# Optimization experiments

Measured on AMD Instinct MI355X. Metric: run time of the kernel, lower is better.

Reference implementation:

```python
import jax, jax.numpy as jnp
import numpy as np

B, L, D, H = 1, 2048, 1024, 16
d = D // H  # head dim = 64


def setup_inputs() -> dict:
    key = jax.random.key(0)
    ks = jax.random.split(key, 8)
    s = 1.0 / np.sqrt(D)
    return {
        "x": jax.random.normal(ks[0], (B, L, D), jnp.float32),
        "Wqkv_w": (jax.random.normal(ks[1], (D, 3 * D), jnp.float32) * s),
        "Wqkv_b": jnp.zeros((3 * D,), jnp.float32),
        "out_w": (jax.random.normal(ks[2], (D, D), jnp.float32) * s),
        "out_b": jnp.zeros((D,), jnp.float32),
        "W_static": jnp.zeros((H, d, d), jnp.float32),
        "Lambda_raw": jax.random.uniform(ks[3], (H, d, d), jnp.float32, -3.0, 3.0),
        "Gamma": jax.random.uniform(ks[4], (H, d, d), jnp.float32, -0.5 / np.sqrt(d), 0.5 / np.sqrt(d)),
        "gate_w1": (jax.random.normal(ks[5], (D, D // 2), jnp.float32) * s),
        "gate_b1": jnp.zeros((D // 2,), jnp.float32),
        "gate_w2": (jax.random.normal(ks[6], (D // 2, H), jnp.float32) * (1.0 / np.sqrt(D // 2))),
        "gate_b2": jnp.zeros((H,), jnp.float32),
    }


def _forward(x, Wqkv_w, Wqkv_b, out_w, out_b, W_static, Lambda_raw, Gamma,
             gate_w1, gate_b1, gate_w2, gate_b2):
    Bb, Ll, Dm = x.shape
    Hh = Gamma.shape[0]
    dd = Dm // Hh
    scale = 1.0 / np.sqrt(dd)

    # qkv projection: (B,L,3D) -> (3, B, H, L, d) layout
    qkv = (x @ Wqkv_w + Wqkv_b).reshape(Bb, Ll, 3, Hh, dd)
    q = jnp.transpose(qkv[:, :, 0], (0, 2, 1, 3))  # (B,H,L,d)
    k = jnp.transpose(qkv[:, :, 1], (0, 2, 1, 3))
    v = jnp.transpose(qkv[:, :, 2], (0, 2, 1, 3))

    # --- softmax branch (causal, additive -10000 mask like the original) ---
    scores = jnp.einsum('bhid,bhjd->bhij', q, k) * scale
    causal_mask = jnp.triu(jnp.full((Ll, Ll), -10000.0, dtype=scores.dtype), 1)
    attn = jax.nn.softmax(scores + causal_mask, axis=-1)
    y_softmax = jnp.einsum('bhij,bhjd->bhid', attn, v)

    # --- STP branch: linear recurrence over time via lax.scan ---
    retention = 1.0 - jax.nn.sigmoid(Lambda_raw)  # (H,d,d)
    k_stp = k * scale

    def step(state, inp):
        q_t, k_t, v_t = inp  # each (B,H,d)
        hebbian = v_t[..., :, None] * k_t[..., None, :]          # (B,H,d,d)
        state = retention * state + Gamma * hebbian              # (B,H,d,d)
        y_t = jnp.einsum('bhij,bhj->bhi', W_static + state, q_t)  # (B,H,d)
        return state, y_t

    state0 = jnp.zeros((Bb, Hh, dd, dd), x.dtype)
    qT = jnp.moveaxis(q, 2, 0)      # (L,B,H,d)
    kT = jnp.moveaxis(k_stp, 2, 0)
    vT = jnp.moveaxis(v, 2, 0)
    _, ys = jax.lax.scan(step, state0, (qT, kT, vT))
    y_stp = jnp.moveaxis(ys, 0, 2)  # (B,H,L,d)

    # --- learned gate: Linear -> GELU(exact) -> Linear -> sigmoid ---
    g = jax.nn.gelu(x @ gate_w1 + gate_b1, approximate=False)
    alpha = jax.nn.sigmoid(g @ gate_w2 + gate_b2)        # (B,L,H)
    alpha = jnp.transpose(alpha, (0, 2, 1))[..., None]   # (B,H,L,1)

    y = alpha * y_softmax + (1.0 - alpha) * y_stp        # (B,H,L,d)
    y = jnp.transpose(y, (0, 2, 1, 3)).reshape(Bb, Ll, Dm)
    return y @ out_w + out_b


def reference(x, Wqkv_w, Wqkv_b, out_w, out_b, W_static, Lambda_raw, Gamma,
              gate_w1, gate_b1, gate_w2, gate_b2):
    return _forward(x, Wqkv_w, Wqkv_b, out_w, out_b, W_static, Lambda_raw,
                    Gamma, gate_w1, gate_b1, gate_w2, gate_b2)
```

## Files before the change

kernel.cpp:

```cpp
#include <hip/hip_runtime.h>
#include <hip/hip_bf16.h>

#define L_SEQ 2048
#define DMODEL 1024
#define NHEAD 16
#define DHEAD 64
#define D3 3072

typedef __attribute__((ext_vector_type(8))) short s8v;
typedef __attribute__((ext_vector_type(4))) float f4v;
typedef unsigned int u32;
#define AS1 __attribute__((address_space(1)))
#define AS3 __attribute__((address_space(3)))

__device__ __forceinline__ short f2bf(float f) {
  __hip_bfloat16 h = __float2bfloat16(f);
  return *reinterpret_cast<short*>(&h);
}
__device__ __forceinline__ float bf2f(short s) {
  return __uint_as_float(((u32)(unsigned short)s) << 16);
}
__device__ __forceinline__ int pack2bf(float lo, float hi) {
  return (int)(((unsigned)(unsigned short)f2bf(hi) << 16) |
               (unsigned)(unsigned short)f2bf(lo));
}

__device__ __forceinline__ void transpose32(const float* __restrict__ W,
    short* __restrict__ Wt, int K, int N, int bx, int by, int tid)
{
  __shared__ float T[32][33];
  int col = tid & 31, rb = tid >> 5;
  #pragma unroll
  for (int it = 0; it < 4; ++it) {
    int r = it * 8 + rb;
    T[r][col] = W[(size_t)(by * 32 + r) * N + bx * 32 + col];
  }
  __syncthreads();
  #pragma unroll
  for (int it = 0; it < 4; ++it) {
    int r = it * 8 + rb;
    Wt[(size_t)(bx * 32 + r) * K + by * 32 + col] = f2bf(T[col][r]);
  }
}

__global__ __launch_bounds__(256) void prep_kernel(
    const float* __restrict__ x, short* __restrict__ xb,
    const float* __restrict__ Wqkv_w, const float* __restrict__ gw1,
    const float* __restrict__ out_w, short* __restrict__ wt_buf,
    short* __restrict__ wtO)
{
  int b = blockIdx.x, tid = threadIdx.x;
  if (b < 2048) {
    int i = (b * 256 + tid) * 4;
    float4 v = *(const float4*)(x + i);
    short4 o;
    o.x = f2bf(v.x); o.y = f2bf(v.y); o.z = f2bf(v.z); o.w = f2bf(v.w);
    *(short4*)(xb + i) = o;
  } else if (b < 5120) {
    int r = b - 2048;
    transpose32(Wqkv_w, wt_buf, 1024, 3072, r % 96, r / 96, tid);
  } else if (b < 5632) {
    int r = b - 5120;
    transpose32(gw1, wt_buf + 3072 * 1024, 1024, 512, r % 16, r / 16, tid);
  } else {
    int r = b - 5632;
    transpose32(out_w, wtO, 1024, 1024, r % 32, r / 32, tid);
  }
}

template<int BM, int BN, int MODE>
__global__ __launch_bounds__(256, 6) void gemm_mfma(
    const short* __restrict__ A, const short* __restrict__ Bt,
    const float* __restrict__ bias, const float* __restrict__ bias2,
    float* __restrict__ C, short* __restrict__ C2,
    short* __restrict__ QbP, short* __restrict__ KbP,
    int M, int N, int K)
{
  constexpr int LA = BM / 64, LB = BN / 64;
  constexpr int WM = BM / 2, WN = BN / 2;
  constexpr int MT = WM / 16, NT = WN / 16;
  __shared__ __align__(16) short As[2][BM * 32];
  __shared__ __align__(16) short Bs[2][BN * 32];
  const int tid = threadIdx.x;
  const int w = tid >> 6, lane = tid & 63;
  const int quad = lane >> 4, c = lane & 15;
  const int m0 = blockIdx.y * BM, n0 = blockIdx.x * BN;
  const int wm = (w & 1) * WM, wn = (w >> 1) * WN;
  f4v acc[MT][NT] = {};

  auto stage = [&](int buf, int k0) {
    #pragma unroll
    for (int it = 0; it < LA; ++it) {
      int off = (it * 256 + tid) * 16;
      int row = off >> 6, colh = (off & 63) >> 1;
      __builtin_amdgcn_global_load_lds(
          (const AS1 u32*)(A + (size_t)(m0 + row) * K + k0 + colh),
          (AS3 u32*)(&As[buf][0] + (off >> 1)), 16, 0, 0);
    }
    #pragma unroll
    for (int it = 0; it < LB; ++it) {
      int off = (it * 256 + tid) * 16;
      int row = off >> 6, colh = (off & 63) >> 1;
      __builtin_amdgcn_global_load_lds(
          (const AS1 u32*)(Bt + (size_t)(n0 + row) * K + k0 + colh),
          (AS3 u32*)(&Bs[buf][0] + (off >> 1)), 16, 0, 0);
    }
  };
  stage(0, 0);
  int cur = 0;
  for (int k0 = 0; k0 < K; k0 += 32) {
    __syncthreads();
    if (k0 + 32 < K) stage(cur ^ 1, k0 + 32);
    s8v af[MT], bf[NT];
    #pragma unroll
    for (int mt = 0; mt < MT; ++mt)
      af[mt] = *(s8v*)&As[cur][(wm + mt * 16 + c) * 32 + quad * 8];
    #pragma unroll
    for (int nt = 0; nt < NT; ++nt)
      bf[nt] = *(s8v*)&Bs[cur][(wn + nt * 16 + c) * 32 + quad * 8];
    #pragma unroll
    for (int mt = 0; mt < MT; ++mt)
      #pragma unroll
      for (int nt = 0; nt < NT; ++nt)
        acc[mt][nt] = __builtin_amdgcn_mfma_f32_16x16x32_bf16(
            af[mt], bf[nt], acc[mt][nt], 0, 0, 0);
    cur ^= 1;
  }
  #pragma unroll
  for (int mt = 0; mt < MT; ++mt)
    #pragma unroll
    for (int r = 0; r < 4; ++r) {
      int m = m0 + wm + mt * 16 + quad * 4 + r;
      #pragma unroll
      for (int nt = 0; nt < NT; ++nt) {
        int n = n0 + wn + nt * 16 + c;
        float v = acc[mt][nt][r];
        if (MODE == 0) {
          C[(size_t)m * N + n] = v + bias[n];
        } else {
          if (n < 2048) {
            float v2 = v + bias[n];
            int hh = (n >> 6) & 15, ee = n & 63;
            short* dst = (n < 1024) ? QbP : KbP;
            dst[((size_t)hh * 2048 + m) * 64 + ee] = f2bf(v2);
          } else if (n < 3072) {
            C[(size_t)m * 1024 + (n - 2048)] = v + bias[n];
          } else {
            float t = v + bias2[n - 3072];
            t = 0.5f * t * (1.0f + erff(t * 0.70710678118654752f));
            C2[(size_t)m * 512 + (n - 3072)] = f2bf(t);
          }
        }
      }
    }
}

__global__ __launch_bounds__(256) void attn_mfma(
    const short* __restrict__ Qb, const short* __restrict__ Kb,
    const short* __restrict__ Vtb, float* __restrict__ O0,
    float* __restrict__ O1, float* __restrict__ ml)
{
  const int bid = blockIdx.x;
  int h, qt, ts, te;
  float *Odst, *mdst, *ldst;
  if (bid < 512) {
    qt = 31 - (bid >> 5);
    int r = bid & 31; h = r >> 1;
    int n = qt + 1, n2 = (n + 1) >> 1;
    if ((r & 1) == 0) {
      ts = 0; te = n2;
      int s = h * 32 + qt;
      Odst = O0 + (size_t)s * 4096; mdst = ml + s * 64; ldst = ml + 32768 + s * 64;
    } else {
      ts = n2; te = n;
      int s = h * 16 + (qt - 16);
      Odst = O1 + (size_t)s * 4096; mdst = ml + 65536 + s * 64; ldst = ml + 81920 + s * 64;
    }
  } else {
    int r = bid - 512; qt = 15 - (r >> 4); h = r & 15; ts = 0; te = qt + 1;
    int s = h * 32 + qt;
    Odst = O0 + (size_t)s * 4096; mdst = ml + s * 64; ldst = ml + 32768 + s * 64;
  }
  const int q0 = qt * 64;
  const int tid = threadIdx.x;
  const int w = tid >> 6, lane = tid & 63;
  const int quad = lane >> 4, c = lane & 15;

  __shared__ __align__(16) char smem[27648];
  short* Ks = (short*)smem;
  short* Vt = Ks + 4608;
  short* Ps = Vt + 4608;
  float* Ob = (float*)smem;

  const int qrow = q0 + w * 16 + c;
  s8v qf[2];
  qf[0] = *(const s8v*)(Qb + ((size_t)h * 2048 + qrow) * 64 + quad * 8);
  qf[1] = *(const s8v*)(Qb + ((size_t)h * 2048 + qrow) * 64 + 32 + quad * 8);

  const int srow = tid >> 3, sc = (tid & 7) * 8;
  int4 pk0, pk1, pv0, pv1;
  auto load_tile = [&](int t0) {
    const short* kbase = Kb + ((size_t)h * 2048 + t0 * 64) * 64;
    const short* vbase = Vtb + (size_t)h * 64 * 2048 + t0 * 64;
    pk0 = *(const int4*)(kbase + (size_t)srow * 64 + sc);
    pk1 = *(const int4*)(kbase + (size_t)(srow + 32) * 64 + sc);
    pv0 = *(const int4*)(vbase + (size_t)srow * 2048 + sc);
    pv1 = *(const int4*)(vbase + (size_t)(srow + 32) * 2048 + sc);
  };
  load_tile(ts);

  f4v o_acc[4] = {};
  float m = -1e30f, l = 0.f;

  for (int t0 = ts; t0 < te; ++t0) {
    __syncthreads();
    *(int4*)&Ks[srow * 72 + sc] = pk0;
    *(int4*)&Ks[(srow + 32) * 72 + sc] = pk1;
    *(int4*)&Vt[srow * 72 + sc] = pv0;
    *(int4*)&Vt[(srow + 32) * 72 + sc] = pv1;
    __syncthreads();
    if (t0 + 1 < te) load_tile(t0 + 1);

    f4v s_acc[4] = {};
    #pragma unroll
    for (int kt = 0; kt < 4; ++kt) {
      #pragma unroll
      for (int kc = 0; kc < 2; ++kc) {
        s8v kf = *(s8v*)&Ks[(kt * 16 + c) * 72 + kc * 32 + quad * 8];
        s_acc[kt] = __builtin_amdgcn_mfma_f32_16x16x32_bf16(kf, qf[kc], s_acc[kt], 0, 0, 0);
      }
    }
    float sv[4][4];
    bool full = (t0 * 64 + 63) <= (q0 + w * 16);
    #pragma unroll
    for (int kt = 0; kt < 4; ++kt)
      #pragma unroll
      for (int r = 0; r < 4; ++r) {
        float s = s_acc[kt][r] * 0.125f;
        if (!full) {
          int key = t0 * 64 + kt * 16 + quad * 4 + r;
          s = (key <= qrow) ? s : -1e30f;
        }
        sv[kt][r] = s;
      }
    float mloc = -1e30f;
    #pragma unroll
    for (int kt = 0; kt < 4; ++kt)
      #pragma unroll
      for (int r = 0; r < 4; ++r) mloc = fmaxf(mloc, sv[kt][r]);
    mloc = fmaxf(mloc, __shfl_xor(mloc, 16));
    mloc = fmaxf(mloc, __shfl_xor(mloc, 32));
    float mnew = fmaxf(fmaxf(m, mloc), -1e20f);
    float alpha = __expf(m - mnew);
    m = mnew;
    float p[4][4], ls = 0.f;
    #pragma unroll
    for (int kt = 0; kt < 4; ++kt)
      #pragma unroll
      for (int r = 0; r < 4; ++r) { p[kt][r] = __expf(sv[kt][r] - mnew); ls += p[kt][r]; }
    ls += __shfl_xor(ls, 16);
    ls += __shfl_xor(ls, 32);
    l = l * alpha + ls;
    #pragma unroll
    for (int mt = 0; mt < 4; ++mt)
      #pragma unroll
      for (int r = 0; r < 4; ++r) o_acc[mt][r] *= alpha;
    short* Pw = Ps + w * 1152;
    #pragma unroll
    for (int kt = 0; kt < 4; ++kt) {
      *(int*)&Pw[c * 72 + kt * 16 + quad * 4]     = pack2bf(p[kt][0], p[kt][1]);
      *(int*)&Pw[c * 72 + kt * 16 + quad * 4 + 2] = pack2bf(p[kt][2], p[kt][3]);
    }
    #pragma unroll
    for (int kc2 = 0; kc2 < 2; ++kc2) {
      s8v pf = *(s8v*)&Pw[c * 72 + kc2 * 32 + quad * 8];
      #pragma unroll
      for (int mt = 0; mt < 4; ++mt) {
        s8v vf = *(s8v*)&Vt[(mt * 16 + c) * 72 + kc2 * 32 + quad * 8];
        o_acc[mt] = __builtin_amdgcn_mfma_f32_16x16x32_bf16(vf, pf, o_acc[mt], 0, 0, 0);
      }
    }
  }

  __syncthreads();
  #pragma unroll
  for (int mt = 0; mt < 4; ++mt)
    #pragma unroll
    for (int r = 0; r < 4; ++r)
      Ob[(w * 16 + c) * 66 + mt * 16 + quad * 4 + r] = o_acc[mt][r];
  if (quad == 0) { mdst[w * 16 + c] = m; ldst[w * 16 + c] = l; }
  __syncthreads();
  for (int i = tid; i < 4096; i += 256)
    Odst[i] = Ob[(i >> 6) * 66 + (i & 63)];
}

__global__ __launch_bounds__(256) void attn_merge(
    const float* __restrict__ O0, const float* __restrict__ O1,
    const float* __restrict__ ml, const float* __restrict__ ystp,
    const float* __restrict__ alpha, short* __restrict__ ycb)
{
  int bid = blockIdx.x;
  int h = bid >> 5, qt = bid & 31;
  int slot0 = h * 32 + qt;
  int tid = threadIdx.x;
  for (int it = 0; it < 16; ++it) {
    int idx = it * 256 + tid;
    int q = idx >> 6, e = idx & 63;
    int gq = qt * 64 + q;
    float oo = O0[(size_t)slot0 * 4096 + idx];
    float m0v = ml[slot0 * 64 + q], l0v = ml[32768 + slot0 * 64 + q];
    float ll;
    if (qt >= 16) {
      int slot1 = h * 16 + (qt - 16);
      float o1 = O1[(size_t)slot1 * 4096 + idx];
      float m1v = ml[65536 + slot1 * 64 + q], l1v = ml[81920 + slot1 * 64 + q];
      float ms = fmaxf(m0v, m1v);
      float w0 = __expf(m0v - ms), w1 = __expf(m1v - ms);
      oo = oo * w0 + o1 * w1;
      ll = l0v * w0 + l1v * w1;
    } else {
      ll = l0v;
    }
    float ys = oo / ll;
    float a = alpha[gq * 16 + h];
    float yst = ystp[((size_t)h * 2048 + gq) * 64 + e];
    ycb[(size_t)gq * 1024 + h * 64 + e] = f2bf(a * ys + (1.f - a) * yst);
  }
}

__global__ __launch_bounds__(256) void stp_local(const float* __restrict__ Vf,
    const short* __restrict__ Kb, const float* __restrict__ Lam,
    const float* __restrict__ Gam, float* __restrict__ states,
    short* __restrict__ Vtb)
{
  int c = blockIdx.x, h = blockIdx.y;
  int tid = threadIdx.x;
  int i = tid >> 2, j0 = (tid & 3) * 16;
  __shared__ float Kc[64][64];
  __shared__ float Vc[64][65];
  for (int idx = tid; idx < 1024; idx += 256) {
    int t = idx >> 4, e4 = (idx & 15) * 4;
    short4 ks = *(const short4*)(Kb + ((size_t)h * 2048 + c * 64 + t) * 64 + e4);
    Kc[t][e4]     = bf2f(ks.x) * 0.125f;
    Kc[t][e4 + 1] = bf2f(ks.y) * 0.125f;
    Kc[t][e4 + 2] = bf2f(ks.z) * 0.125f;
    Kc[t][e4 + 3] = bf2f(ks.w) * 0.125f;
    float4 vv = *(const float4*)(Vf + (size_t)(c * 64 + t) * 1024 + h * 64 + e4);
    Vc[t][e4] = vv.x; Vc[t][e4 + 1] = vv.y; Vc[t][e4 + 2] = vv.z; Vc[t][e4 + 3] = vv.w;
  }
  float r[16], g[16], s[16];
  #pragma unroll
  for (int e = 0; e < 16; ++e) {
    int idx = h * 4096 + i * 64 + j0 + e;
    r[e] = 1.f / (1.f + expf(Lam[idx]));
    g[e] = Gam[idx];
    s[e] = 0.f;
  }
  __syncthreads();
  for (int idx = tid; idx < 2048; idx += 256) {
    int dim = idx >> 5, k2 = idx & 31;
    *(int*)&Vtb[((size_t)h * 64 + dim) * 2048 + c * 64 + k2 * 2] =
        pack2bf(Vc[k2 * 2][dim], Vc[k2 * 2 + 1][dim]);
  }
  for (int t = 0; t < 64; ++t) {
    float v = Vc[t][i];
    #pragma unroll
    for (int e = 0; e < 16; ++e)
      s[e] = r[e] * s[e] + g[e] * (v * Kc[t][j0 + e]);
  }
  #pragma unroll
  for (int e = 0; e < 16; ++e)
    states[((size_t)h * 32 + c) * 4096 + i * 64 + j0 + e] = s[e];
}

__global__ __launch_bounds__(256) void stp_scan(const float* __restrict__ Lam,
                                                float* __restrict__ states)
{
  int gid = blockIdx.x * 256 + threadIdx.x;
  float r = 1.f / (1.f + expf(Lam[gid]));
  float r64 = r;
  #pragma unroll
  for (int q = 0; q < 6; ++q) r64 *= r64;
  int h = gid >> 12, low = gid & 4095;
  const size_t base = (size_t)h * 32 * 4096 + low;
  float v[32];
  #pragma unroll
  for (int c = 0; c < 32; ++c) v[c] = states[base + (size_t)c * 4096];
  float acc = 0.f;
  #pragma unroll
  for (int c = 0; c < 32; ++c) {
    float d = v[c];
    v[c] = acc;
    acc = r64 * acc + d;
  }
  #pragma unroll
  for (int c = 0; c < 32; ++c) states[base + (size_t)c * 4096] = v[c];
}

__global__ __launch_bounds__(256) void stp_out(const float* __restrict__ Vf,
    const short* __restrict__ Kb, const short* __restrict__ Qb,
    const float* __restrict__ Lam, const float* __restrict__ Gam,
    const float* __restrict__ Wst, const float* __restrict__ states,
    float* __restrict__ ystp)
{
  int c = blockIdx.x, h = blockIdx.y;
  int tid = threadIdx.x;
  int i = tid >> 2, j0 = (tid & 3) * 16;
  __shared__ float Kc[64][64];
  __shared__ float Vc[64][64];
  __shared__ float Qc[64][64];
  for (int idx = tid; idx < 1024; idx += 256) {
    int t = idx >> 4, e4 = (idx & 15) * 4;
    size_t bo = ((size_t)h * 2048 + c * 64 + t) * 64 + e4;
    short4 ks = *(const short4*)(Kb + bo);
    short4 qs = *(const short4*)(Qb + bo);
    Kc[t][e4]     = bf2f(ks.x) * 0.125f;
    Kc[t][e4 + 1] = bf2f(ks.y) * 0.125f;
    Kc[t][e4 + 2] = bf2f(ks.z) * 0.125f;
    Kc[t][e4 + 3] = bf2f(ks.w) * 0.125f;
    Qc[t][e4]     = bf2f(qs.x);
    Qc[t][e4 + 1] = bf2f(qs.y);
    Qc[t][e4 + 2] = bf2f(qs.z);
    Qc[t][e4 + 3] = bf2f(qs.w);
    float4 vv = *(const float4*)(Vf + (size_t)(c * 64 + t) * 1024 + h * 64 + e4);
    Vc[t][e4] = vv.x; Vc[t][e4 + 1] = vv.y; Vc[t][e4 + 2] = vv.z; Vc[t][e4 + 3] = vv.w;
  }
  float r[16], g[16], s[16], w[16];
  #pragma unroll
  for (int e = 0; e < 16; ++e) {
    int idx = h * 4096 + i * 64 + j0 + e;
    r[e] = 1.f / (1.f + expf(Lam[idx]));
    g[e] = Gam[idx];
    w[e] = Wst[idx];
    s[e] = states[((size_t)h * 32 + c) * 4096 + i * 64 + j0 + e];
  }
  __syncthreads();
  for (int t = 0; t < 64; ++t) {
    float v = Vc[t][i];
    float y = 0.f;
    #pragma unroll
    for (int e = 0; e < 16; ++e) {
      s[e] = r[e] * s[e] + g[e] * (v * Kc[t][j0 + e]);
      y += (w[e] + s[e]) * Qc[t][j0 + e];
    }
    y += __shfl_xor(y, 1);
    y += __shfl_xor(y, 2);
    if ((tid & 3) == 0)
      ystp[((size_t)h * L_SEQ + c * 64 + t) * 64 + i] = y;
  }
}

__global__ __launch_bounds__(256) void gate2_kernel(const short* __restrict__ g_bf,
    const float* __restrict__ w2, const float* __restrict__ b2,
    float* __restrict__ alpha)
{
  int tid = threadIdx.x;
  int gid = blockIdx.x * 16 + (tid >> 4);
  int sub = tid & 15;
  int l = gid >> 4, h = gid & 15;
  const short* grow = g_bf + (size_t)l * 512 + sub * 32;
  float acc = 0.f;
  #pragma unroll
  for (int c2 = 0; c2 < 32; c2 += 2) {
    u32 pk = *(const u32*)(grow + c2);
    float g0 = __uint_as_float(pk << 16);
    float g1 = __uint_as_float(pk & 0xffff0000u);
    int cb = sub * 32 + c2;
    acc += g0 * w2[cb * 16 + h] + g1 * w2[(cb + 1) * 16 + h];
  }
  acc += __shfl_xor(acc, 1);
  acc += __shfl_xor(acc, 2);
  acc += __shfl_xor(acc, 4);
  acc += __shfl_xor(acc, 8);
  if (sub == 0) alpha[gid] = 1.f / (1.f + expf(-(acc + b2[h])));
}

extern "C" void kernel_launch(void* const* d_in, const int* in_sizes, int n_in,
                              void* d_out, int out_size, void* d_ws, size_t ws_size,
                              hipStream_t stream) {
  (void)in_sizes; (void)n_in; (void)out_size; (void)ws_size;
  const float* x      = (const float*)d_in[0];
  const float* Wqkv_w = (const float*)d_in[1];
  const float* Wqkv_b = (const float*)d_in[2];
  const float* out_w  = (const float*)d_in[3];
  const float* out_b  = (const float*)d_in[4];
  const float* W_st   = (const float*)d_in[5];
  const float* Lam    = (const float*)d_in[6];
  const float* Gam    = (const float*)d_in[7];
  const float* gw1    = (const float*)d_in[8];
  const float* gb1    = (const float*)d_in[9];
  const float* gw2    = (const float*)d_in[10];
  const float* gb2    = (const float*)d_in[11];

  float* ws     = (float*)d_ws;
  float* Vf     = ws;
  float* O0buf  = ws + 2097152;
  float* ystp   = ws + 4194304;
  float* states = ws + 6291456;
  float* ovl    = ws + 8388608;
  float* alpha  = ws + 12058624;
  float* ml     = ws + 12091392;
  short* Qb     = (short*)(ws + 12189696);
  short* Kb     = Qb + 2097152;
  short* wtO    = (short*)(ws + 14286848);
  short* xb     = (short*)ovl;
  short* wt_buf = (short*)(ovl + 1048576);
  short* g_bf   = (short*)(ovl + 2883584);
  short* Vtb    = (short*)ovl;
  float* O1buf  = states;
  short* ycb    = (short*)(states + 1048576);

  prep_kernel<<<dim3(6656), 256, 0, stream>>>(x, xb, Wqkv_w, gw1, out_w, wt_buf, wtO);
  gemm_mfma<64, 64, 2><<<dim3(56, 32), 256, 0, stream>>>(
      xb, wt_buf, Wqkv_b, gb1, Vf, g_bf, Qb, Kb, 2048, 3584, 1024);
  gate2_kernel<<<dim3(2048), 256, 0, stream>>>(g_bf, gw2, gb2, alpha);
  stp_local<<<dim3(32, 16), 256, 0, stream>>>(Vf, Kb, Lam, Gam, states, Vtb);
  stp_scan<<<dim3(256), 256, 0, stream>>>(Lam, states);
  stp_out<<<dim3(32, 16), 256, 0, stream>>>(Vf, Kb, Qb, Lam, Gam, W_st, states, ystp);
  attn_mfma<<<dim3(768), 256, 0, stream>>>(Qb, Kb, Vtb, O0buf, O1buf, ml);
  attn_merge<<<dim3(512), 256, 0, stream>>>(O0buf, O1buf, ml, ystp, alpha, ycb);
  gemm_mfma<64, 64, 0><<<dim3(16, 32), 256, 0, stream>>>(
      ycb, wtO, out_b, nullptr, (float*)d_out, nullptr, nullptr, nullptr, 2048, 1024, 1024);
}
```

Before: 277.2 us.

## Split attention key range into up to three pieces and split-K the output GEMM

```diff
diff --git a/kernel.cpp b/kernel.cpp
--- a/kernel.cpp
+++ b/kernel.cpp
@@ -84,7 +84,17 @@
   const int tid = threadIdx.x;
   const int w = tid >> 6, lane = tid & 63;
   const int quad = lane >> 4, c = lane & 15;
-  const int m0 = blockIdx.y * BM, n0 = blockIdx.x * BN;
+  int n0, kb, ke;
+  size_t cofs = 0;
+  if (MODE == 3) {
+    n0 = (blockIdx.x & 15) * BN;
+    int kh = blockIdx.x >> 4;
+    kb = kh * (K / 2); ke = kb + K / 2;
+    cofs = (size_t)kh * M * N;
+  } else {
+    n0 = blockIdx.x * BN; kb = 0; ke = K;
+  }
+  const int m0 = blockIdx.y * BM;
   const int wm = (w & 1) * WM, wn = (w >> 1) * WN;
   f4v acc[MT][NT] = {};
 
@@ -106,11 +116,11 @@
           (AS3 u32*)(&Bs[buf][0] + (off >> 1)), 16, 0, 0);
     }
   };
-  stage(0, 0);
+  stage(0, kb);
   int cur = 0;
-  for (int k0 = 0; k0 < K; k0 += 32) {
+  for (int k0 = kb; k0 < ke; k0 += 32) {
     __syncthreads();
-    if (k0 + 32 < K) stage(cur ^ 1, k0 + 32);
+    if (k0 + 32 < ke) stage(cur ^ 1, k0 + 32);
     s8v af[MT], bf[NT];
     #pragma unroll
     for (int mt = 0; mt < MT; ++mt)
@@ -135,8 +145,8 @@
       for (int nt = 0; nt < NT; ++nt) {
         int n = n0 + wn + nt * 16 + c;
         float v = acc[mt][nt][r];
-        if (MODE == 0) {
-          C[(size_t)m * N + n] = v + bias[n];
+        if (MODE == 3) {
+          C[cofs + (size_t)m * N + n] = v;
         } else {
           if (n < 2048) {
             float v2 = v + bias[n];
@@ -155,32 +165,42 @@
     }
 }
 
+__global__ __launch_bounds__(256) void splitk_add(const float* __restrict__ Cp,
+    const float* __restrict__ bias, float* __restrict__ out)
+{
+  int i = (blockIdx.x * 256 + threadIdx.x) * 4;
+  float4 a = *(const float4*)(Cp + i);
+  float4 b = *(const float4*)(Cp + 2097152 + i);
+  float4 bs = *(const float4*)(bias + (i & 1023));
+  float4 o;
+  o.x = a.x + b.x + bs.x; o.y = a.y + b.y + bs.y;
+  o.z = a.z + b.z + bs.z; o.w = a.w + b.w + bs.w;
+  *(float4*)(out + i) = o;
+}
+
+__device__ __forceinline__ int piece_slot(int qt, int h, int p) {
+  if (qt >= 16) return (qt - 16) * 48 + h * 3 + p;
+  if (qt >= 8)  return 768 + (qt - 8) * 32 + h * 2 + p;
+  return 1024 + qt * 16 + h;
+}
+
 __global__ __launch_bounds__(256) void attn_mfma(
     const short* __restrict__ Qb, const short* __restrict__ Kb,
-    const short* __restrict__ Vtb, float* __restrict__ O0,
-    float* __restrict__ O1, float* __restrict__ ml)
+    const short* __restrict__ Vtb, float* __restrict__ Opart,
+    float* __restrict__ mpart, float* __restrict__ lpart)
 {
   const int bid = blockIdx.x;
-  int h, qt, ts, te;
-  float *Odst, *mdst, *ldst;
-  if (bid < 512) {
-    qt = 31 - (bid >> 5);
-    int r = bid & 31; h = r >> 1;
-    int n = qt + 1, n2 = (n + 1) >> 1;
-    if ((r & 1) == 0) {
-      ts = 0; te = n2;
-      int s = h * 32 + qt;
-      Odst = O0 + (size_t)s * 4096; mdst = ml + s * 64; ldst = ml + 32768 + s * 64;
-    } else {
-      ts = n2; te = n;
-      int s = h * 16 + (qt - 16);
-      Odst = O1 + (size_t)s * 4096; mdst = ml + 65536 + s * 64; ldst = ml + 81920 + s * 64;
-    }
-  } else {
-    int r = bid - 512; qt = 15 - (r >> 4); h = r & 15; ts = 0; te = qt + 1;
-    int s = h * 32 + qt;
-    Odst = O0 + (size_t)s * 4096; mdst = ml + s * 64; ldst = ml + 32768 + s * 64;
-  }
+  int h, qt, p, np;
+  if (bid < 768)       { int j = bid;        qt = 31 - j / 48; int r = j % 48; h = r / 3; p = r % 3; np = 3; }
+  else if (bid < 1024) { int j = bid - 768;  qt = 15 - j / 32; int r = j % 32; h = r >> 1; p = r & 1; np = 2; }
+  else                 { int j = bid - 1024; qt = 7 - (j >> 4); h = j & 15; p = 0; np = 1; }
+  const int n = qt + 1;
+  const int ts = (p * n) / np, te = ((p + 1) * n) / np;
+  const int ps = piece_slot(qt, h, p);
+  float* Odst = Opart + (size_t)ps * 4096;
+  float* mdst = mpart + ps * 64;
+  float* ldst = lpart + ps * 64;
+
   const int q0 = qt * 64;
   const int tid = threadIdx.x;
   const int w = tid >> 6, lane = tid & 63;
@@ -253,11 +273,11 @@
     float mnew = fmaxf(fmaxf(m, mloc), -1e20f);
     float alpha = __expf(m - mnew);
     m = mnew;
-    float p[4][4], ls = 0.f;
+    float pv[4][4], ls = 0.f;
     #pragma unroll
     for (int kt = 0; kt < 4; ++kt)
       #pragma unroll
-      for (int r = 0; r < 4; ++r) { p[kt][r] = __expf(sv[kt][r] - mnew); ls += p[kt][r]; }
+      for (int r = 0; r < 4; ++r) { pv[kt][r] = __expf(sv[kt][r] - mnew); ls += pv[kt][r]; }
     ls += __shfl_xor(ls, 16);
     ls += __shfl_xor(ls, 32);
     l = l * alpha + ls;
@@ -268,8 +288,8 @@
     short* Pw = Ps + w * 1152;
     #pragma unroll
     for (int kt = 0; kt < 4; ++kt) {
-      *(int*)&Pw[c * 72 + kt * 16 + quad * 4]     = pack2bf(p[kt][0], p[kt][1]);
-      *(int*)&Pw[c * 72 + kt * 16 + quad * 4 + 2] = pack2bf(p[kt][2], p[kt][3]);
+      *(int*)&Pw[c * 72 + kt * 16 + quad * 4]     = pack2bf(pv[kt][0], pv[kt][1]);
+      *(int*)&Pw[c * 72 + kt * 16 + quad * 4 + 2] = pack2bf(pv[kt][2], pv[kt][3]);
     }
     #pragma unroll
     for (int kc2 = 0; kc2 < 2; ++kc2) {
@@ -295,31 +315,27 @@
 }
 
 __global__ __launch_bounds__(256) void attn_merge(
-    const float* __restrict__ O0, const float* __restrict__ O1,
-    const float* __restrict__ ml, const float* __restrict__ ystp,
+    const float* __restrict__ Opart, const float* __restrict__ mpart,
+    const float* __restrict__ lpart, const float* __restrict__ ystp,
     const float* __restrict__ alpha, short* __restrict__ ycb)
 {
   int bid = blockIdx.x;
   int h = bid >> 5, qt = bid & 31;
-  int slot0 = h * 32 + qt;
+  int np = (qt >= 16) ? 3 : ((qt >= 8) ? 2 : 1);
+  int ps0 = piece_slot(qt, h, 0);
   int tid = threadIdx.x;
   for (int it = 0; it < 16; ++it) {
     int idx = it * 256 + tid;
     int q = idx >> 6, e = idx & 63;
     int gq = qt * 64 + q;
-    float oo = O0[(size_t)slot0 * 4096 + idx];
-    float m0v = ml[slot0 * 64 + q], l0v = ml[32768 + slot0 * 64 + q];
-    float ll;
-    if (qt >= 16) {
-      int slot1 = h * 16 + (qt - 16);
-      float o1 = O1[(size_t)slot1 * 4096 + idx];
-      float m1v = ml[65536 + slot1 * 64 + q], l1v = ml[81920 + slot1 * 64 + q];
-      float ms = fmaxf(m0v, m1v);
-      float w0 = __expf(m0v - ms), w1 = __expf(m1v - ms);
-      oo = oo * w0 + o1 * w1;
-      ll = l0v * w0 + l1v * w1;
-    } else {
-      ll = l0v;
+    float ms = mpart[ps0 * 64 + q];
+    for (int p2 = 1; p2 < np; ++p2)
+      ms = fmaxf(ms, mpart[(ps0 + p2) * 64 + q]);
+    float oo = 0.f, ll = 0.f;
+    for (int p2 = 0; p2 < np; ++p2) {
+      float wp = __expf(mpart[(ps0 + p2) * 64 + q] - ms);
+      oo += Opart[(size_t)(ps0 + p2) * 4096 + idx] * wp;
+      ll += lpart[(ps0 + p2) * 64 + q] * wp;
     }
     float ys = oo / ll;
     float a = alpha[gq * 16 + h];
@@ -494,21 +510,21 @@
 
   float* ws     = (float*)d_ws;
   float* Vf     = ws;
-  float* O0buf  = ws + 2097152;
-  float* ystp   = ws + 4194304;
-  float* states = ws + 6291456;
-  float* ovl    = ws + 8388608;
-  float* alpha  = ws + 12058624;
-  float* ml     = ws + 12091392;
-  short* Qb     = (short*)(ws + 12189696);
-  short* Kb     = Qb + 2097152;
-  short* wtO    = (short*)(ws + 14286848);
-  short* xb     = (short*)ovl;
-  short* wt_buf = (short*)(ovl + 1048576);
-  short* g_bf   = (short*)(ovl + 2883584);
-  short* Vtb    = (short*)ovl;
-  float* O1buf  = states;
-  short* ycb    = (short*)(states + 1048576);
+  float* ystp   = ws + 2097152;
+  float* states = ws + 4194304;
+  short* xb     = (short*)(ws + 6291456);
+  short* wt_buf = (short*)(ws + 7340032);
+  short* g_bf   = (short*)(ws + 9175040);
+  float* alpha  = ws + 9699328;
+  short* Qb     = (short*)(ws + 9732096);
+  short* Kb     = (short*)(ws + 10780672);
+  short* wtO    = (short*)(ws + 11829248);
+  short* Vtb    = (short*)(ws + 12353536);
+  short* ycb    = (short*)(ws + 13402112);
+  float* Opart  = ws + 14450688;
+  float* mpart  = ws + 19169280;
+  float* lpart  = ws + 19243008;
+  float* Cpart  = ws + 19316736;
 
   prep_kernel<<<dim3(6656), 256, 0, stream>>>(x, xb, Wqkv_w, gw1, out_w, wt_buf, wtO);
   gemm_mfma<64, 64, 2><<<dim3(56, 32), 256, 0, stream>>>(
@@ -517,8 +533,9 @@
   stp_local<<<dim3(32, 16), 256, 0, stream>>>(Vf, Kb, Lam, Gam, states, Vtb);
   stp_scan<<<dim3(256), 256, 0, stream>>>(Lam, states);
   stp_out<<<dim3(32, 16), 256, 0, stream>>>(Vf, Kb, Qb, Lam, Gam, W_st, states, ystp);
-  attn_mfma<<<dim3(768), 256, 0, stream>>>(Qb, Kb, Vtb, O0buf, O1buf, ml);
-  attn_merge<<<dim3(512), 256, 0, stream>>>(O0buf, O1buf, ml, ystp, alpha, ycb);
-  gemm_mfma<64, 64, 0><<<dim3(16, 32), 256, 0, stream>>>(
-      ycb, wtO, out_b, nullptr, (float*)d_out, nullptr, nullptr, nullptr, 2048, 1024, 1024);
-}
+  attn_mfma<<<dim3(1152), 256, 0, stream>>>(Qb, Kb, Vtb, Opart, mpart, lpart);
+  attn_merge<<<dim3(512), 256, 0, stream>>>(Opart, mpart, lpart, ystp, alpha, ycb);
+  gemm_mfma<64, 64, 3><<<dim3(32, 32), 256, 0, stream>>>(
+      ycb, wtO, nullptr, nullptr, Cpart, nullptr, nullptr, nullptr, 2048, 1024, 1024);
+  splitk_add<<<dim3(2048), 256, 0, stream>>>(Cpart, out_b, (float*)d_out);
+}
```

Result: slower. 286.7 us (+3.4%).
